# Kernel optimization log

Measured on AMD Instinct MI355X. Metric: run time of the kernel, lower is better.

The kernel has to match this reference:

```python
import jax, jax.numpy as jnp
import numpy as np

NF, NLOC, NNEI = 4, 2048, 64
EMBED, PAIR_DIM, H = 128, 64, 8
HD = EMBED // H
EPS = 1e-5

def _ln(x, g, b):
    m = x.mean(-1, keepdims=True)
    v = ((x - m) ** 2).mean(-1, keepdims=True)
    return (x - m) * jax.lax.rsqrt(v + EPS) * g + b

def setup_inputs() -> dict:
    key = jax.random.key(0)
    ks = jax.random.split(key, 12)
    inp = {
        "query": jax.random.normal(ks[0], (NF, NLOC, EMBED), jnp.float32),
        "pair": jax.random.normal(ks[1], (NF, NLOC, NNEI, PAIR_DIM), jnp.float32),
        "nlist": jax.random.randint(ks[2], (NF, NLOC, NNEI), 0, NLOC, jnp.int64),
        "delta_pos": jax.random.normal(ks[3], (NF, NLOC, NNEI, 3), jnp.float32),
        "attn_mask": jnp.zeros((NF, H, NLOC, NNEI), jnp.float32),
        "ln_g": jnp.ones((EMBED,), jnp.float32),
        "ln_b": jnp.zeros((EMBED,), jnp.float32),
        "pn_g": jnp.ones((PAIR_DIM,), jnp.float32),
        "pn_b": jnp.zeros((PAIR_DIM,), jnp.float32),
        "Wq": jax.random.normal(ks[4], (EMBED, EMBED), jnp.float32) * (EMBED ** -0.5),
        "Wk": jax.random.normal(ks[5], (EMBED, EMBED), jnp.float32) * (EMBED ** -0.5),
        "Wv": jax.random.normal(ks[6], (EMBED, EMBED), jnp.float32) * (EMBED ** -0.5),
        "Wbias": jax.random.normal(ks[7], (H, PAIR_DIM), jnp.float32) * (PAIR_DIM ** -0.5),
        "bbias": jnp.zeros((H,), jnp.float32),
        "Wforce": jax.random.normal(ks[8], (1, EMBED), jnp.float32) * (EMBED ** -0.5),
    }
    return inp

def reference(query, pair, nlist, delta_pos, attn_mask,
              ln_g, ln_b, pn_g, pn_b, Wq, Wk, Wv, Wbias, bbias, Wforce):
    nf, nloc, _ = query.shape
    nnei = nlist.shape[-1]
    qn = _ln(query, ln_g, ln_b)            # [f,l,e]
    pn = _ln(pair, pn_g, pn_b)             # [f,l,n,p]
    scaling = HD ** -0.5
    q = (qn @ Wq.T).reshape(nf, nloc, H, HD) * scaling       # [f,l,h,d]
    k = qn @ Wk.T                                            # [f,l,e]
    v = qn @ Wv.T
    idx = nlist.reshape(nf, -1)[..., None]                   # [f,l*n,1]
    kg = jnp.take_along_axis(k, idx, axis=1).reshape(nf, nloc, nnei, H, HD)
    vg = jnp.take_along_axis(v, idx, axis=1).reshape(nf, nloc, nnei, H, HD)
    attn = jnp.einsum('flhd,flnhd->fhln', q, kg)             # [f,h,l,n]
    bias = jnp.einsum('flnp,hp->fhln', pn, Wbias) + bbias[None, :, None, None]
    probs = jax.nn.softmax(attn + attn_mask + bias, axis=-1)  # dropout off (eval)
    # rotate by delta_pos and contract with v over neighbors
    x = jnp.einsum('fhln,flnc,flnhd->flchd', probs, delta_pos, vg)
    x = x.reshape(nf, nloc, 3, EMBED)
    force = (x @ Wforce.T).squeeze(-1)                       # [f,l,3]
    return force
```

## Files before the change

kernel.cpp:

```cpp
#include <hip/hip_runtime.h>

#define NFR   4
#define NLOCC 2048
#define NNEIN 64
#define EMB   128
#define PDIM  64
#define NH    8
#define LNEPS 1e-5f
#define NROW  (NFR*NLOCC)

#define WS_Q   0
#define WS_K   (NROW*EMB)
#define WS_FV  (2*NROW*EMB)
#define WS_WVF (2*NROW*EMB + NROW*NH)
#define WS_G   (WS_WVF + NH*EMB)
#define WS_SG  (WS_G + NH*PDIM)

__device__ __forceinline__ void fma4(float4& acc, const float4 a, const float4 b) {
    acc.x = fmaf(a.x, b.x, acc.x);
    acc.y = fmaf(a.y, b.y, acc.y);
    acc.z = fmaf(a.z, b.z, acc.z);
    acc.w = fmaf(a.w, b.w, acc.w);
}
__device__ __forceinline__ void fma4s(float4& acc, const float s, const float4 b) {
    acc.x = fmaf(s, b.x, acc.x);
    acc.y = fmaf(s, b.y, acc.y);
    acc.z = fmaf(s, b.z, acc.z);
    acc.w = fmaf(s, b.w, acc.w);
}
__device__ __forceinline__ float hsum4(const float4 a) {
    return (a.x + a.y) + (a.z + a.w);
}
__device__ __forceinline__ float dot4(const float4 a, const float4 b) {
    return fmaf(a.x, b.x, fmaf(a.y, b.y, fmaf(a.z, b.z, a.w * b.w)));
}
__device__ __forceinline__ float4 scale4(const float4 a, const float s) {
    return make_float4(a.x*s, a.y*s, a.z*s, a.w*s);
}

__global__ __launch_bounds__(256) void precompute_kernel(
    const float* __restrict__ pn_g, const float* __restrict__ pn_b,
    const float* __restrict__ Wbias, const float* __restrict__ bbias,
    const float* __restrict__ Wv, const float* __restrict__ Wforce,
    float* __restrict__ ws)
{
    const int t = threadIdx.x;
    {
        const int h  = t >> 5;
        const int e0 = (t & 31) * 4;
        float4 acc = make_float4(0.f, 0.f, 0.f, 0.f);
        #pragma unroll
        for (int d = 0; d < 16; ++d) {
            const float wf = Wforce[h*16 + d];
            const float4 wv = *(const float4*)(Wv + (size_t)(h*16 + d)*EMB + e0);
            fma4s(acc, wf, wv);
        }
        *(float4*)(ws + WS_WVF + (size_t)h*EMB + e0) = acc;
    }
    for (int idx = t; idx < NH*PDIM; idx += 256) {
        const int h = idx >> 6, p = idx & 63;
        ws[WS_G + idx] = pn_g[p] * Wbias[h*PDIM + p];
    }
    if (t < NH) {
        float sg = 0.f, c = 0.f;
        #pragma unroll 8
        for (int p = 0; p < PDIM; ++p) {
            const float wb = Wbias[t*PDIM + p];
            sg = fmaf(pn_g[p], wb, sg);
            c  = fmaf(pn_b[p], wb, c);
        }
        ws[WS_SG + t]      = sg;
        ws[WS_SG + NH + t] = c + bbias[t];
    }
}

__global__ __launch_bounds__(256, 2) void qkfv_kernel(
    const float* __restrict__ query,
    const float* __restrict__ ln_g, const float* __restrict__ ln_b,
    const float* __restrict__ Wq, const float* __restrict__ Wk,
    float* __restrict__ ws)
{
    __shared__ float gb_s[2][EMB];
    __shared__ float qn_s[16*132];
    __shared__ float wt_s[2][16*132];
    const int t = threadIdx.x;
    const int rowbase = blockIdx.x * 16;

    if (t < 64) {
        const float* src = (t < 32) ? ln_g : ln_b;
        ((float4*)gb_s[t >> 5])[t & 31] = ((const float4*)src)[t & 31];
    }

    const int r   = t >> 4;
    const int seg = t & 15;
    float4 x0 = ((const float4*)query)[(size_t)(rowbase + r)*32 + seg*2 + 0];
    float4 x1 = ((const float4*)query)[(size_t)(rowbase + r)*32 + seg*2 + 1];
    float s  = (x0.x + x0.y) + (x0.z + x0.w) + (x1.x + x1.y) + (x1.z + x1.w);
    float ss = x0.x*x0.x + x0.y*x0.y + x0.z*x0.z + x0.w*x0.w
             + x1.x*x1.x + x1.y*x1.y + x1.z*x1.z + x1.w*x1.w;
    #pragma unroll
    for (int m = 1; m < 16; m <<= 1) {
        s  += __shfl_xor(s,  m, 64);
        ss += __shfl_xor(ss, m, 64);
    }
    const float mean = s * (1.0f / 128.0f);
    const float var  = ss * (1.0f / 128.0f) - mean * mean;
    const float rstd = rsqrtf(var + LNEPS);
    __syncthreads();

    {
        const int c0 = seg * 8;
        float4 o0, o1;
        o0.x = (x0.x - mean)*rstd*gb_s[0][c0+0] + gb_s[1][c0+0];
        o0.y = (x0.y - mean)*rstd*gb_s[0][c0+1] + gb_s[1][c0+1];
        o0.z = (x0.z - mean)*rstd*gb_s[0][c0+2] + gb_s[1][c0+2];
        o0.w = (x0.w - mean)*rstd*gb_s[0][c0+3] + gb_s[1][c0+3];
        o1.x = (x1.x - mean)*rstd*gb_s[0][c0+4] + gb_s[1][c0+4];
        o1.y = (x1.y - mean)*rstd*gb_s[0][c0+5] + gb_s[1][c0+5];
        o1.z = (x1.z - mean)*rstd*gb_s[0][c0+6] + gb_s[1][c0+6];
        o1.w = (x1.w - mean)*rstd*gb_s[0][c0+7] + gb_s[1][c0+7];
        ((float4*)qn_s)[r*33 + seg*2 + 0] = o0;
        ((float4*)qn_s)[r*33 + seg*2 + 1] = o1;
    }
    __syncthreads();

    const int rp = t >> 5;
    const int r0 = rp * 2;
    const int cq = t & 31;
    const int sc0 = t >> 2;
    const int si0 = t & 3;
    const float4* qn4 = (const float4*)qn_s;

    for (int w = 0; w < 2; ++w) {
        const float4* W4 = (const float4*)((w == 0) ? Wq : Wk);
        float4 acc0 = make_float4(0.f,0.f,0.f,0.f);
        float4 acc1 = make_float4(0.f,0.f,0.f,0.f);
        {
            float4 g0 = W4[(size_t)sc0*32 + si0];
            float4 g1 = W4[(size_t)(sc0+64)*32 + si0];
            float* wt = wt_s[0];
            wt[(si0*4+0)*132 + sc0] = g0.x; wt[(si0*4+1)*132 + sc0] = g0.y;
            wt[(si0*4+2)*132 + sc0] = g0.z; wt[(si0*4+3)*132 + sc0] = g0.w;
            wt[(si0*4+0)*132 + sc0+64] = g1.x; wt[(si0*4+1)*132 + sc0+64] = g1.y;
            wt[(si0*4+2)*132 + sc0+64] = g1.z; wt[(si0*4+3)*132 + sc0+64] = g1.w;
        }
        __syncthreads();
        #pragma unroll
        for (int tau = 0; tau < 8; ++tau) {
            const int buf = tau & 1;
            float4 ng0, ng1;
            if (tau < 7) {
                ng0 = W4[(size_t)sc0*32 + (tau+1)*4 + si0];
                ng1 = W4[(size_t)(sc0+64)*32 + (tau+1)*4 + si0];
            }
            const float4* wt4 = (const float4*)wt_s[buf];
            #pragma unroll
            for (int e4 = 0; e4 < 4; ++e4) {
                float4 a0 = qn4[r0*33 + tau*4 + e4];
                float4 a1 = qn4[(r0+1)*33 + tau*4 + e4];
                const float* a0p = (const float*)&a0;
                const float* a1p = (const float*)&a1;
                #pragma unroll
                for (int ee = 0; ee < 4; ++ee) {
                    const float4 wv = wt4[(e4*4+ee)*33 + cq];
                    fma4s(acc0, a0p[ee], wv);
                    fma4s(acc1, a1p[ee], wv);
                }
            }
            if (tau < 7) {
                float* wt = wt_s[buf ^ 1];
                wt[(si0*4+0)*132 + sc0] = ng0.x; wt[(si0*4+1)*132 + sc0] = ng0.y;
                wt[(si0*4+2)*132 + sc0] = ng0.z; wt[(si0*4+3)*132 + sc0] = ng0.w;
                wt[(si0*4+0)*132 + sc0+64] = ng1.x; wt[(si0*4+1)*132 + sc0+64] = ng1.y;
                wt[(si0*4+2)*132 + sc0+64] = ng1.z; wt[(si0*4+3)*132 + sc0+64] = ng1.w;
            }
            __syncthreads();
        }
        const float sc = (w == 0) ? 0.25f : 1.0f;
        float4* dst = (float4*)(ws + (w == 0 ? WS_Q : WS_K));
        dst[(size_t)(rowbase + r0)*32 + cq]     = scale4(acc0, sc);
        dst[(size_t)(rowbase + r0 + 1)*32 + cq] = scale4(acc1, sc);
    }

    if (t < 128) {
        const int rr = t >> 3, h = t & 7;
        const float4* wvf4 = (const float4*)(ws + WS_WVF + (size_t)h*EMB);
        float4 acc = make_float4(0.f,0.f,0.f,0.f);
        #pragma unroll
        for (int ch = 0; ch < 32; ++ch)
            fma4(acc, qn4[rr*33 + ch], wvf4[ch]);
        ws[WS_FV + (size_t)(rowbase + rr)*NH + h] = hsum4(acc);
    }
}

__global__ __launch_bounds__(256, 4) void attn_force_kernel(
    const float* __restrict__ pair, const int* __restrict__ nlist,
    const float* __restrict__ delta_pos, const float* __restrict__ attn_mask,
    const float* __restrict__ ws, float* __restrict__ out)
{
    __shared__ float4 pair_s4[64*17];
    __shared__ float  logit_s[NNEIN*9];
    __shared__ float4 G_s4[128];
    __shared__ float  dp_s[192];
    __shared__ float  fpart[4][3];

    const int t    = threadIdx.x;
    const int bid  = blockIdx.x;
    const int fr   = bid >> 11;
    const int l    = bid & 2047;
    const int w    = t >> 6;
    const int lane = t & 63;
    const int half = lane >> 5;
    const int c    = lane & 31;
    const int n    = t >> 2;
    const int sub  = t & 3;
    const int h0   = sub * 2, h1 = h0 + 1;
    const int i32  = lane & 31;
    const int hh   = t >> 5;

    {
        const float4* p4 = (const float4*)pair + (size_t)bid*1024;
        #pragma unroll
        for (int i = 0; i < 4; ++i) {
            const int ci   = i*256 + t;
            const float4 v = p4[ci];
            pair_s4[(ci >> 4)*17 + (ci & 15)] = v;
        }
    }
    const int jv = nlist[(size_t)bid*NNEIN + lane];
    const float4 q4c = ((const float4*)(ws + WS_Q))[(size_t)bid*32 + c];

    const float mask0 = attn_mask[((size_t)(fr*NH + h0)*NLOCC + l)*NNEIN + n];
    const float mask1 = attn_mask[((size_t)(fr*NH + h1)*NLOCC + l)*NNEIN + n];
    const float sg0 = ws[WS_SG + h0],      sg1 = ws[WS_SG + h1];
    const float cc0 = ws[WS_SG + NH + h0], cc1 = ws[WS_SG + NH + h1];

    if (t < 128) G_s4[t] = ((const float4*)(ws + WS_G))[t];
    if (t < 48)  ((float4*)dp_s)[t] = ((const float4*)(delta_pos + (size_t)bid*192))[t];

    const int    jn  = __shfl(jv, n & 63, 64);
    const float2 fv2 = ((const float2*)(ws + WS_FV + ((size_t)(fr << 11) + jn)*NH))[sub];

    {
        const float4* k4 = (const float4*)(ws + WS_K) + (size_t)(fr << 11)*32;
        int jr[8];
        #pragma unroll
        for (int i = 0; i < 8; ++i)
            jr[i] = __shfl(jv, (w << 4) | (i << 1) | half, 64);
        float4 kkA[4], kkB[4];
        #pragma unroll
        for (int i = 0; i < 4; ++i) kkA[i] = k4[(size_t)jr[i]*32 + c];
        #pragma unroll
        for (int i = 0; i < 4; ++i) kkB[i] = k4[(size_t)jr[4+i]*32 + c];
        float p[8];
        #pragma unroll
        for (int i = 0; i < 4; ++i) p[i]     = dot4(kkA[i], q4c);
        #pragma unroll
        for (int i = 0; i < 4; ++i) p[4 + i] = dot4(kkB[i], q4c);
        #pragma unroll
        for (int i = 0; i < 8; ++i) {
            float pp = p[i];
            pp += __shfl_xor(pp, 1, 64);
            pp += __shfl_xor(pp, 2, 64);
            if ((c & 3) == 0)
                logit_s[((w << 4) | (i << 1) | half)*9 + (c >> 2)] = pp;
        }
    }
    __syncthreads();

    {
        const float4 pr0 = pair_s4[n*17 + sub*4 + 0];
        const float4 pr1 = pair_s4[n*17 + sub*4 + 1];
        const float4 pr2 = pair_s4[n*17 + sub*4 + 2];
        const float4 pr3 = pair_s4[n*17 + sub*4 + 3];
        float s  = hsum4(pr0) + hsum4(pr1) + hsum4(pr2) + hsum4(pr3);
        float ss = dot4(pr0, pr0) + dot4(pr1, pr1) + dot4(pr2, pr2) + dot4(pr3, pr3);
        s  += __shfl_xor(s, 1, 64);  s  += __shfl_xor(s, 2, 64);
        ss += __shfl_xor(ss, 1, 64); ss += __shfl_xor(ss, 2, 64);
        const float mean = s * (1.0f / 64.0f);
        const float var  = ss * (1.0f / 64.0f) - mean * mean;
        const float rstd = rsqrtf(var + LNEPS);

        float d[NH];
        #pragma unroll
        for (int h = 0; h < NH; ++h) d[h] = 0.f;
        const float4 prq[4] = {pr0, pr1, pr2, pr3};
        #pragma unroll
        for (int q = 0; q < 4; ++q) {
            #pragma unroll
            for (int h = 0; h < NH; ++h)
                d[h] += dot4(prq[q], G_s4[h*16 + sub*4 + q]);
        }
        #pragma unroll
        for (int h = 0; h < NH; ++h) {
            d[h] += __shfl_xor(d[h], 1, 64);
            d[h] += __shfl_xor(d[h], 2, 64);
        }
        const float b0 = rstd*(d[h0] - mean*sg0) + cc0 + mask0;
        const float b1 = rstd*(d[h1] - mean*sg1) + cc1 + mask1;
        logit_s[n*9 + h0] += b0;
        logit_s[n*9 + h1] += b1;
    }
    __syncthreads();

    {
        float a = logit_s[i32*9 + hh], b = logit_s[(i32 + 32)*9 + hh];
        float m = fmaxf(a, b);
        #pragma unroll
        for (int mm = 16; mm >= 1; mm >>= 1) m = fmaxf(m, __shfl_xor(m, mm, 64));
        float ea = __expf(a - m), eb = __expf(b - m);
        float sum = ea + eb;
        #pragma unroll
        for (int mm = 16; mm >= 1; mm >>= 1) sum += __shfl_xor(sum, mm, 64);
        const float inv = 1.0f / sum;
        logit_s[i32*9 + hh]        = ea * inv;
        logit_s[(i32 + 32)*9 + hh] = eb * inv;
    }
    __syncthreads();

    {
        const float p0 = logit_s[n*9 + h0];
        const float p1 = logit_s[n*9 + h1];
        float sn = p0*fv2.x + p1*fv2.y;
        sn += __shfl_xor(sn, 1, 64);
        sn += __shfl_xor(sn, 2, 64);
        float fc = (sub < 3) ? sn * dp_s[n*3 + sub] : 0.f;
        #pragma unroll
        for (int mm = 4; mm <= 32; mm <<= 1)
            fc += __shfl_xor(fc, mm, 64);
        if (lane < 3) fpart[w][lane] = fc;
    }
    __syncthreads();

    if (t < 3)
        out[(size_t)bid*3 + t] = fpart[0][t] + fpart[1][t] + fpart[2][t] + fpart[3][t];
}

extern "C" void kernel_launch(void* const* d_in, const int* in_sizes, int n_in,
                              void* d_out, int out_size, void* d_ws, size_t ws_size,
                              hipStream_t stream) {
    const float* query     = (const float*)d_in[0];
    const float* pair      = (const float*)d_in[1];
    const int*   nlist     = (const int*)d_in[2];
    const float* delta_pos = (const float*)d_in[3];
    const float* attn_mask = (const float*)d_in[4];
    const float* ln_g      = (const float*)d_in[5];
    const float* ln_b      = (const float*)d_in[6];
    const float* pn_g      = (const float*)d_in[7];
    const float* pn_b      = (const float*)d_in[8];
    const float* Wq        = (const float*)d_in[9];
    const float* Wk        = (const float*)d_in[10];
    const float* Wv        = (const float*)d_in[11];
    const float* Wbias     = (const float*)d_in[12];
    const float* bbias     = (const float*)d_in[13];
    const float* Wforce    = (const float*)d_in[14];
    float* out = (float*)d_out;
    float* ws  = (float*)d_ws;

    precompute_kernel<<<1, 256, 0, stream>>>(pn_g, pn_b, Wbias, bbias, Wv, Wforce, ws);
    qkfv_kernel<<<512, 256, 0, stream>>>(query, ln_g, ln_b, Wq, Wk, ws);
    attn_force_kernel<<<NROW, 256, 0, stream>>>(pair, nlist, delta_pos, attn_mask, ws, out);
}
```

Baseline: 260.0 us.

## Fold weight precompute into consumer kernels and fuse softmax with force reduction

Removes the single-block precompute kernel. Each qkfv block now recomputes the Wv·Wforce product into shared memory, and each attention block rebuilds the pair-bias weight products and per-head constants itself. The softmax stage now multiplies the probabilities by the gathered per-neighbor values and reduces against delta_pos in the same pass, which drops one barrier and a shared-memory round trip. In exchange every block does redundant weight math (8192 attention blocks each recompute G and the head constants) and qkfv blocks do extra global reads of Wv.

```diff
diff --git a/kernel.cpp b/kernel.cpp
--- a/kernel.cpp
+++ b/kernel.cpp
@@ -12,9 +12,6 @@
 #define WS_Q   0
 #define WS_K   (NROW*EMB)
 #define WS_FV  (2*NROW*EMB)
-#define WS_WVF (2*NROW*EMB + NROW*NH)
-#define WS_G   (WS_WVF + NH*EMB)
-#define WS_SG  (WS_G + NH*PDIM)
 
 __device__ __forceinline__ void fma4(float4& acc, const float4 a, const float4 b) {
     acc.x = fmaf(a.x, b.x, acc.x);
@@ -38,57 +35,35 @@
     return make_float4(a.x*s, a.y*s, a.z*s, a.w*s);
 }
 
-__global__ __launch_bounds__(256) void precompute_kernel(
-    const float* __restrict__ pn_g, const float* __restrict__ pn_b,
-    const float* __restrict__ Wbias, const float* __restrict__ bbias,
-    const float* __restrict__ Wv, const float* __restrict__ Wforce,
-    float* __restrict__ ws)
-{
-    const int t = threadIdx.x;
-    {
-        const int h  = t >> 5;
-        const int e0 = (t & 31) * 4;
-        float4 acc = make_float4(0.f, 0.f, 0.f, 0.f);
-        #pragma unroll
-        for (int d = 0; d < 16; ++d) {
-            const float wf = Wforce[h*16 + d];
-            const float4 wv = *(const float4*)(Wv + (size_t)(h*16 + d)*EMB + e0);
-            fma4s(acc, wf, wv);
-        }
-        *(float4*)(ws + WS_WVF + (size_t)h*EMB + e0) = acc;
-    }
-    for (int idx = t; idx < NH*PDIM; idx += 256) {
-        const int h = idx >> 6, p = idx & 63;
-        ws[WS_G + idx] = pn_g[p] * Wbias[h*PDIM + p];
-    }
-    if (t < NH) {
-        float sg = 0.f, c = 0.f;
-        #pragma unroll 8
-        for (int p = 0; p < PDIM; ++p) {
-            const float wb = Wbias[t*PDIM + p];
-            sg = fmaf(pn_g[p], wb, sg);
-            c  = fmaf(pn_b[p], wb, c);
-        }
-        ws[WS_SG + t]      = sg;
-        ws[WS_SG + NH + t] = c + bbias[t];
-    }
-}
-
 __global__ __launch_bounds__(256, 2) void qkfv_kernel(
     const float* __restrict__ query,
     const float* __restrict__ ln_g, const float* __restrict__ ln_b,
     const float* __restrict__ Wq, const float* __restrict__ Wk,
+    const float* __restrict__ Wv, const float* __restrict__ Wforce,
     float* __restrict__ ws)
 {
-    __shared__ float gb_s[2][EMB];
-    __shared__ float qn_s[16*132];
-    __shared__ float wt_s[2][16*132];
+    __shared__ float  gb_s[2][EMB];
+    __shared__ float  qn_s[16*132];
+    __shared__ float  wt_s[2][16*132];
+    __shared__ float4 wvf_s4[8*33];
     const int t = threadIdx.x;
     const int rowbase = blockIdx.x * 16;
 
     if (t < 64) {
         const float* src = (t < 32) ? ln_g : ln_b;
         ((float4*)gb_s[t >> 5])[t & 31] = ((const float4*)src)[t & 31];
+    }
+
+    {
+        const int h = t >> 5, ch = t & 31;
+        float4 acc = make_float4(0.f, 0.f, 0.f, 0.f);
+        #pragma unroll
+        for (int d = 0; d < 16; ++d) {
+            const float wf = Wforce[h*16 + d];
+            const float4 wv = ((const float4*)(Wv + (size_t)(h*16 + d)*EMB))[ch];
+            fma4s(acc, wf, wv);
+        }
+        wvf_s4[h*33 + ch] = acc;
     }
 
     const int r   = t >> 4;
@@ -184,11 +159,10 @@
 
     if (t < 128) {
         const int rr = t >> 3, h = t & 7;
-        const float4* wvf4 = (const float4*)(ws + WS_WVF + (size_t)h*EMB);
         float4 acc = make_float4(0.f,0.f,0.f,0.f);
         #pragma unroll
         for (int ch = 0; ch < 32; ++ch)
-            fma4(acc, qn4[rr*33 + ch], wvf4[ch]);
+            fma4(acc, qn4[rr*33 + ch], wvf_s4[h*33 + ch]);
         ws[WS_FV + (size_t)(rowbase + rr)*NH + h] = hsum4(acc);
     }
 }
@@ -196,11 +170,15 @@
 __global__ __launch_bounds__(256, 4) void attn_force_kernel(
     const float* __restrict__ pair, const int* __restrict__ nlist,
     const float* __restrict__ delta_pos, const float* __restrict__ attn_mask,
+    const float* __restrict__ pn_g, const float* __restrict__ pn_b,
+    const float* __restrict__ Wbias, const float* __restrict__ bbias,
     const float* __restrict__ ws, float* __restrict__ out)
 {
     __shared__ float4 pair_s4[64*17];
     __shared__ float  logit_s[NNEIN*9];
     __shared__ float4 G_s4[128];
+    __shared__ float  csg_s[16];
+    __shared__ float  fv_s[NNEIN*9];
     __shared__ float  dp_s[192];
     __shared__ float  fpart[4][3];
 
@@ -232,14 +210,35 @@
 
     const float mask0 = attn_mask[((size_t)(fr*NH + h0)*NLOCC + l)*NNEIN + n];
     const float mask1 = attn_mask[((size_t)(fr*NH + h1)*NLOCC + l)*NNEIN + n];
-    const float sg0 = ws[WS_SG + h0],      sg1 = ws[WS_SG + h1];
-    const float cc0 = ws[WS_SG + NH + h0], cc1 = ws[WS_SG + NH + h1];
-
-    if (t < 128) G_s4[t] = ((const float4*)(ws + WS_G))[t];
-    if (t < 48)  ((float4*)dp_s)[t] = ((const float4*)(delta_pos + (size_t)bid*192))[t];
-
-    const int    jn  = __shfl(jv, n & 63, 64);
-    const float2 fv2 = ((const float2*)(ws + WS_FV + ((size_t)(fr << 11) + jn)*NH))[sub];
+
+    if (t < 128) {
+        const int p4i = t & 15;
+        const float4 wb4 = ((const float4*)Wbias)[t];
+        const float4 pg4 = ((const float4*)pn_g)[p4i];
+        G_s4[t] = make_float4(wb4.x*pg4.x, wb4.y*pg4.y, wb4.z*pg4.z, wb4.w*pg4.w);
+    } else if (t < 192) {
+        const int h = (t - 128) >> 3, s8 = (t - 128) & 7;
+        float sg = 0.f, cb = 0.f;
+        #pragma unroll
+        for (int k = 0; k < 8; ++k) {
+            const int p = s8*8 + k;
+            const float wb = Wbias[h*PDIM + p];
+            sg = fmaf(pn_g[p], wb, sg);
+            cb = fmaf(pn_b[p], wb, cb);
+        }
+        sg += __shfl_xor(sg, 1, 64); sg += __shfl_xor(sg, 2, 64); sg += __shfl_xor(sg, 4, 64);
+        cb += __shfl_xor(cb, 1, 64); cb += __shfl_xor(cb, 2, 64); cb += __shfl_xor(cb, 4, 64);
+        if (s8 == 0) { csg_s[h] = sg; csg_s[8 + h] = cb + bbias[h]; }
+    } else if (t < 240) {
+        ((float4*)dp_s)[t - 192] = ((const float4*)(delta_pos + (size_t)bid*192))[t - 192];
+    }
+
+    {
+        const int    jn  = __shfl(jv, n & 63, 64);
+        const float2 fv2 = ((const float2*)(ws + WS_FV + ((size_t)(fr << 11) + jn)*NH))[sub];
+        fv_s[n*9 + h0] = fv2.x;
+        fv_s[n*9 + h1] = fv2.y;
+    }
 
     {
         const float4* k4 = (const float4*)(ws + WS_K) + (size_t)(fr << 11)*32;
@@ -296,39 +295,39 @@
             d[h] += __shfl_xor(d[h], 1, 64);
             d[h] += __shfl_xor(d[h], 2, 64);
         }
-        const float b0 = rstd*(d[h0] - mean*sg0) + cc0 + mask0;
-        const float b1 = rstd*(d[h1] - mean*sg1) + cc1 + mask1;
-        logit_s[n*9 + h0] += b0;
-        logit_s[n*9 + h1] += b1;
-    }
-    __syncthreads();
-
-    {
-        float a = logit_s[i32*9 + hh], b = logit_s[(i32 + 32)*9 + hh];
+        logit_s[n*9 + h0] += rstd*(d[h0] - mean*csg_s[h0]) + csg_s[8 + h0] + mask0;
+        logit_s[n*9 + h1] += rstd*(d[h1] - mean*csg_s[h1]) + csg_s[8 + h1] + mask1;
+    }
+    __syncthreads();
+
+    {
+        const float a = logit_s[i32*9 + hh], b = logit_s[(i32 + 32)*9 + hh];
         float m = fmaxf(a, b);
         #pragma unroll
         for (int mm = 16; mm >= 1; mm >>= 1) m = fmaxf(m, __shfl_xor(m, mm, 64));
-        float ea = __expf(a - m), eb = __expf(b - m);
+        const float ea = __expf(a - m), eb = __expf(b - m);
         float sum = ea + eb;
         #pragma unroll
         for (int mm = 16; mm >= 1; mm >>= 1) sum += __shfl_xor(sum, mm, 64);
         const float inv = 1.0f / sum;
-        logit_s[i32*9 + hh]        = ea * inv;
-        logit_s[(i32 + 32)*9 + hh] = eb * inv;
-    }
-    __syncthreads();
-
-    {
-        const float p0 = logit_s[n*9 + h0];
-        const float p1 = logit_s[n*9 + h1];
-        float sn = p0*fv2.x + p1*fv2.y;
-        sn += __shfl_xor(sn, 1, 64);
-        sn += __shfl_xor(sn, 2, 64);
-        float fc = (sub < 3) ? sn * dp_s[n*3 + sub] : 0.f;
-        #pragma unroll
-        for (int mm = 4; mm <= 32; mm <<= 1)
-            fc += __shfl_xor(fc, mm, 64);
-        if (lane < 3) fpart[w][lane] = fc;
+        float ca = ea * inv * fv_s[i32*9 + hh];
+        float cb = eb * inv * fv_s[(i32 + 32)*9 + hh];
+        ca += __shfl_xor(ca, 32, 64);
+        cb += __shfl_xor(cb, 32, 64);
+        const float dpax = dp_s[i32*3 + 0],        dpay = dp_s[i32*3 + 1],        dpaz = dp_s[i32*3 + 2];
+        const float dpbx = dp_s[(i32+32)*3 + 0],   dpby = dp_s[(i32+32)*3 + 1],   dpbz = dp_s[(i32+32)*3 + 2];
+        float f0 = ca*dpax + cb*dpbx;
+        float f1 = ca*dpay + cb*dpby;
+        float f2 = ca*dpaz + cb*dpbz;
+        #pragma unroll
+        for (int mm = 1; mm <= 16; mm <<= 1) {
+            f0 += __shfl_xor(f0, mm, 64);
+            f1 += __shfl_xor(f1, mm, 64);
+            f2 += __shfl_xor(f2, mm, 64);
+        }
+        if (lane == 0) {
+            fpart[w][0] = f0; fpart[w][1] = f1; fpart[w][2] = f2;
+        }
     }
     __syncthreads();
 
@@ -357,7 +356,7 @@
     float* out = (float*)d_out;
     float* ws  = (float*)d_ws;
 
-    precompute_kernel<<<1, 256, 0, stream>>>(pn_g, pn_b, Wbias, bbias, Wv, Wforce, ws);
-    qkfv_kernel<<<512, 256, 0, stream>>>(query, ln_g, ln_b, Wq, Wk, ws);
-    attn_force_kernel<<<NROW, 256, 0, stream>>>(pair, nlist, delta_pos, attn_mask, ws, out);
-}
+    qkfv_kernel<<<512, 256, 0, stream>>>(query, ln_g, ln_b, Wq, Wk, Wv, Wforce, ws);
+    attn_force_kernel<<<NROW, 256, 0, stream>>>(pair, nlist, delta_pos, attn_mask,
+                                                pn_g, pn_b, Wbias, bbias, ws, out);
+}
```

Result: faster. 253.5 us (-2.5%).
